# Performance work log

Measured on AMD Instinct MI355X. Metric: run time of the kernel, lower is better.

## Reference

```python
import jax, jax.numpy as jnp
import numpy as np

DIM = 768
NUM_HEADS = 12
HEAD_DIM = DIM // NUM_HEADS
SCALE = HEAD_DIM ** -0.5
B, N = 8, 1024


def setup_inputs() -> dict:
    key = jax.random.key(0)
    k1, k2, k3, k4 = jax.random.split(key, 4)
    s = 1.0 / np.sqrt(DIM)
    return {
        "x": jax.random.normal(k1, (B, N, DIM), dtype=jnp.float32),
        "w_qkv": jax.random.normal(k2, (DIM, 3 * DIM), dtype=jnp.float32) * s,  # qkv_bias=False
        "w_proj": jax.random.normal(k3, (DIM, DIM), dtype=jnp.float32) * s,
        "b_proj": jax.random.normal(k4, (DIM,), dtype=jnp.float32) * 0.01,
    }


def reference(x, w_qkv, w_proj, b_proj):
    Bb, Nn, C = x.shape
    qkv = x @ w_qkv  # [B, N, 3C]
    qkv = qkv.reshape(Bb, Nn, 3, NUM_HEADS, HEAD_DIM)
    q = qkv[:, :, 0].transpose(0, 2, 1, 3)  # [B, H, N, d]
    k = qkv[:, :, 1].transpose(0, 2, 1, 3)
    v = qkv[:, :, 2].transpose(0, 2, 1, 3)
    attn = jnp.einsum("bhqd,bhkd->bhqk", q, k) * SCALE
    attn = jax.nn.softmax(attn, axis=-1)  # dropout p=0 -> identity
    out = jnp.einsum("bhqk,bhkd->bhqd", attn, v)
    out = out.transpose(0, 2, 1, 3).reshape(Bb, Nn, C)
    return out @ w_proj + b_proj
```

## Files before the change

### kernel.cpp

```cpp
#include <hip/hip_runtime.h>
#include <stdint.h>

typedef __attribute__((ext_vector_type(8))) __bf16 bf16x8;
typedef __attribute__((ext_vector_type(8))) unsigned short u16x8;
typedef __attribute__((ext_vector_type(4))) unsigned short u16x4;
typedef __attribute__((ext_vector_type(4))) short s16x4;
typedef __attribute__((ext_vector_type(4))) float f32x4;

typedef unsigned int u32_as1 __attribute__((address_space(1)));
typedef unsigned int u32_as3 __attribute__((address_space(3)));

__device__ __forceinline__ unsigned short f2bf(float f) {
  unsigned int u = __float_as_uint(f);
  u += 0x7fffu + ((u >> 16) & 1u);
  return (unsigned short)(u >> 16);
}

__device__ __forceinline__ bf16x8 ld_frag(const unsigned short* p) {
  return __builtin_bit_cast(bf16x8, *(const u16x8*)p);
}

__device__ __forceinline__ f32x4 mfma16(s16x4 a, s16x4 b, f32x4 c) {
#if __has_builtin(__builtin_amdgcn_mfma_f32_16x16x16bf16_1k)
  return __builtin_amdgcn_mfma_f32_16x16x16bf16_1k(a, b, c, 0, 0, 0);
#elif __has_builtin(__builtin_amdgcn_mfma_f32_16x16x16_bf16_1k)
  return __builtin_amdgcn_mfma_f32_16x16x16_bf16_1k(a, b, c, 0, 0, 0);
#else
  asm volatile("v_mfma_f32_16x16x16_bf16 %0, %1, %2, %0"
               : "+v"(c) : "v"(a), "v"(b));
  return c;
#endif
}

__device__ __forceinline__ float fast_exp2(float x) {
#if __has_builtin(__builtin_amdgcn_exp2f)
  return __builtin_amdgcn_exp2f(x);
#else
  return exp2f(x);
#endif
}

__device__ __forceinline__ void async16(const void* g, void* l) {
  const u32_as1* gp = (const u32_as1*)(uintptr_t)g;
  u32_as3* lp = (u32_as3*)(uintptr_t)l;
  __builtin_amdgcn_global_load_lds(gp, lp, 16, 0, 0);
}

template <int N> __device__ __forceinline__ void wait_vmcnt() {
  if constexpr (N == 0)      asm volatile("s_waitcnt vmcnt(0)" ::: "memory");
  else if constexpr (N == 4) asm volatile("s_waitcnt vmcnt(4)" ::: "memory");
  else if constexpr (N == 6) asm volatile("s_waitcnt vmcnt(6)" ::: "memory");
}

__global__ __launch_bounds__(256) void prep_kernel(
    const float* __restrict__ x, const float* __restrict__ w_qkv,
    const float* __restrict__ w_proj, u16x4* __restrict__ x_bf,
    unsigned short* __restrict__ wqkvT, unsigned short* __restrict__ wprojT) {
  const int bid = blockIdx.x;
  const int t = threadIdx.x;
  if (bid < 6144) {
    const int i = bid * 256 + t;
    float4 v = ((const float4*)x)[i];
    u16x4 o;
    o[0] = f2bf(v.x); o[1] = f2bf(v.y); o[2] = f2bf(v.z); o[3] = f2bf(v.w);
    x_bf[i] = o;
    return;
  }
  __shared__ float tile[32][33];
  const float* w; unsigned short* wt; int N, bx, by;
  if (bid < 6144 + 1728) { const int r = bid - 6144; w = w_qkv; wt = wqkvT; N = 2304; bx = r % 72; by = r / 72; }
  else                   { const int r = bid - 7872; w = w_proj; wt = wprojT; N = 768; bx = r % 24; by = r / 24; }
  const int n0 = bx * 32, k0 = by * 32;
  const int tx = t & 31, ty = t >> 5;
#pragma unroll
  for (int r = 0; r < 4; r++)
    tile[ty + r * 8][tx] = w[(k0 + ty + r * 8) * N + n0 + tx];
  __syncthreads();
#pragma unroll
  for (int r = 0; r < 4; r++)
    wt[(n0 + ty + r * 8) * 768 + k0 + tx] = f2bf(tile[tx][ty + r * 8]);
}

template <int EPI>
__global__ __launch_bounds__(512, 2) void gemm256(
    const unsigned short* __restrict__ A, const unsigned short* __restrict__ Bt,
    unsigned short* __restrict__ qb, unsigned short* __restrict__ kb,
    unsigned short* __restrict__ vtb, float* __restrict__ outp,
    const float* __restrict__ bias) {
  constexpr int NKT = 12;
  constexpr int SSH = 24576;
  __shared__ unsigned short smem[3 * SSH];

  const int t = threadIdx.x;
  const int lane = t & 63, w = t >> 6;
  const int quad = lane >> 4, l15 = lane & 15;
  const int wm = w >> 1, wn = w & 1;

  const int bid = blockIdx.x;
  const int xcd = bid & 7, slot = bid >> 3;
  const int m0 = (xcd * 4 + (slot & 3)) * 256;
  const int n0 = (slot >> 2) * 128;

  int aoff[4][2], boff[4][2];
#pragma unroll
  for (int i = 0; i < 4; i++) {
    const int row = wm * 64 + i * 16 + l15;
    const int rs = row & 7;
#pragma unroll
    for (int kk = 0; kk < 2; kk++)
      aoff[i][kk] = row * 64 + (((kk * 4 + quad) ^ rs) << 3);
  }
#pragma unroll
  for (int j = 0; j < 4; j++) {
    const int row = wn * 64 + j * 16 + l15;
    const int rs = row & 7;
#pragma unroll
    for (int kk = 0; kk < 2; kk++)
      boff[j][kk] = 16384 + row * 64 + (((kk * 4 + quad) ^ rs) << 3);
  }

  const int srow = t >> 3;
  const int gch = ((t & 7) ^ (srow & 7)) << 3;
  const unsigned short* Ags = A + (m0 + srow) * 768 + gch;
  const unsigned short* Bgs = Bt + (n0 + srow) * 768 + gch;

  f32x4 acc[4][4];
  const f32x4 fzero = {0.f, 0.f, 0.f, 0.f};
#pragma unroll
  for (int i = 0; i < 4; i++)
#pragma unroll
    for (int j = 0; j < 4; j++) acc[i][j] = fzero;

  auto stage = [&](int kt, int part) {
    unsigned short* s = smem + (kt % 3) * SSH + t * 8;
    const int ko = kt * 64;
    if (part == 0) {
      async16(Ags + ko, s);
      async16(Ags + 49152 + ko, s + 4096);
      async16(Ags + 98304 + ko, s + 8192);
    } else {
      async16(Ags + 147456 + ko, s + 12288);
      async16(Bgs + ko, s + 16384);
      async16(Bgs + 49152 + ko, s + 20480);
    }
  };

  stage(0, 0); stage(0, 1);
  stage(1, 0); stage(1, 1);

#pragma unroll
  for (int kt = 0; kt < NKT; ++kt) {
    const unsigned short* S = smem + (kt % 3) * SSH;
#pragma unroll
    for (int ph = 0; ph < 2; ++ph) {
      if (ph == 0) {
        if (kt < NKT - 1) wait_vmcnt<6>();
        else              wait_vmcnt<0>();
      }
      __builtin_amdgcn_s_barrier();

      bf16x8 af[4], bf[4];
#pragma unroll
      for (int i = 0; i < 4; i++) af[i] = ld_frag(S + aoff[i][ph]);
#pragma unroll
      for (int j = 0; j < 4; j++) bf[j] = ld_frag(S + boff[j][ph]);

      if (kt + 2 < NKT) stage(kt + 2, ph);

      __builtin_amdgcn_s_setprio(1);
#pragma unroll
      for (int i = 0; i < 4; i++)
#pragma unroll
        for (int j = 0; j < 4; j++)
          acc[i][j] = __builtin_amdgcn_mfma_f32_16x16x32_bf16(af[i], bf[j], acc[i][j], 0, 0, 0);
      __builtin_amdgcn_s_setprio(0);
    }
  }

#pragma unroll
  for (int i = 0; i < 4; i++) {
    const int gmb = m0 + wm * 64 + i * 16 + quad * 4;
#pragma unroll
    for (int j = 0; j < 4; j++) {
      const int gc = n0 + wn * 64 + j * 16 + l15;
#pragma unroll
      for (int r = 0; r < 4; r++) {
        const int gm = gmb + r;
        float v = acc[i][j][r];
        if (EPI == 0) {
          const int b = gm >> 10, tok = gm & 1023;
          const int which = (gc >= 1536) ? 2 : (gc >= 768 ? 1 : 0);
          const int rem = gc - which * 768;
          const int h = rem >> 6, d = rem & 63;
          const int bh = b * 12 + h;
          const unsigned short bv = f2bf(v);
          if (which == 0)      qb[(bh << 16) + (tok << 6) + d] = bv;
          else if (which == 1) kb[(bh << 16) + (tok << 6) + d] = bv;
          else                 vtb[(bh << 16) + (d << 10) + tok] = bv;
        } else {
          outp[gm * 768 + gc] = v + bias[gc];
        }
      }
    }
  }
}

#define SWZC(row, c) (((row) << 6) + ((((c) + (row)) & 7) << 3))
#define C2 0.1803368801111244f

__global__ __launch_bounds__(256, 3) void attn_kernel(
    const unsigned short* __restrict__ qb, const unsigned short* __restrict__ kb,
    const unsigned short* __restrict__ vtb, unsigned short* __restrict__ aout) {
  __shared__ unsigned short smem[3 * 8192];

  const int t = threadIdx.x;
  const int lane = t & 63, w = t >> 6;
  const int quad = lane >> 4, l15 = lane & 15;
  const int bh = blockIdx.x;
  const int b = bh / 12, h = bh - b * 12;
  const int q0 = blockIdx.y * 128;
  const int base = bh << 16;

  bf16x8 qf[2][2];
#pragma unroll
  for (int qt = 0; qt < 2; qt++)
#pragma unroll
    for (int s = 0; s < 2; s++)
      qf[qt][s] = ld_frag(qb + base + ((q0 + w * 32 + qt * 16 + l15) << 6) +
                          s * 32 + quad * 8);

  f32x4 oacc[4][2];
  const f32x4 fzero = {0.f, 0.f, 0.f, 0.f};
#pragma unroll
  for (int dt = 0; dt < 4; dt++) { oacc[dt][0] = fzero; oacc[dt][1] = fzero; }
  float lsum0 = 0.f, lsum1 = 0.f;

  const int srow = t >> 3, schk = t & 7;
  const int c0 = ((schk - srow) & 7) * 8;
  const int c1 = ((schk - (srow + 32)) & 7) * 8;

  auto fillkv = [&](int tile, int buf) {
    const int kv0 = tile * 64;
    unsigned short* Ks = smem + buf * 8192;
    unsigned short* Vts = Ks + 4096;
    async16(kb + base + ((kv0 + srow) << 6) + c0, Ks + t * 8);
    async16(kb + base + ((kv0 + srow + 32) << 6) + c1, Ks + 2048 + t * 8);
    async16(vtb + base + (srow << 10) + kv0 + c0, Vts + t * 8);
    async16(vtb + base + ((srow + 32) << 10) + kv0 + c1, Vts + 2048 + t * 8);
  };

  fillkv(0, 0);
  fillkv(1, 1);
  int cur = 0;
  for (int it = 0; it < 16; ++it) {
    if (it < 15) wait_vmcnt<4>(); else wait_vmcnt<0>();
    asm volatile("s_barrier" ::: "memory");
    if (it + 2 < 16) {
      int tgt = cur + 2; if (tgt >= 3) tgt -= 3;
      fillkv(it + 2, tgt);
    }
    const unsigned short* Ks = smem + cur * 8192;
    const unsigned short* Vts = Ks + 4096;

    f32x4 st[4][2];
#pragma unroll
    for (int tc = 0; tc < 4; tc++) { st[tc][0] = fzero; st[tc][1] = fzero; }
#pragma unroll
    for (int s = 0; s < 2; s++) {
#pragma unroll
      for (int tc = 0; tc < 4; tc++) {
        const bf16x8 kf = ld_frag(Ks + SWZC(tc * 16 + l15, s * 4 + quad));
        st[tc][0] = __builtin_amdgcn_mfma_f32_16x16x32_bf16(kf, qf[0][s], st[tc][0], 0, 0, 0);
        st[tc][1] = __builtin_amdgcn_mfma_f32_16x16x32_bf16(kf, qf[1][s], st[tc][1], 0, 0, 0);
      }
    }

    s16x4 pf[4][2];
#pragma unroll
    for (int tc = 0; tc < 4; tc++) {
#pragma unroll
      for (int qt = 0; qt < 2; qt++) {
        const float p0 = fast_exp2(st[tc][qt][0] * C2);
        const float p1 = fast_exp2(st[tc][qt][1] * C2);
        const float p2 = fast_exp2(st[tc][qt][2] * C2);
        const float p3 = fast_exp2(st[tc][qt][3] * C2);
        const float ps = (p0 + p1) + (p2 + p3);
        if (qt == 0) lsum0 += ps; else lsum1 += ps;
        s16x4 pk;
        pk[0] = (short)f2bf(p0); pk[1] = (short)f2bf(p1);
        pk[2] = (short)f2bf(p2); pk[3] = (short)f2bf(p3);
        pf[tc][qt] = pk;
      }
    }

#pragma unroll
    for (int tc = 0; tc < 4; tc++) {
#pragma unroll
      for (int dt = 0; dt < 4; dt++) {
        const int row = dt * 16 + l15;
        const int addr = (row << 6) + ((((tc * 2 + (quad >> 1)) + row) & 7) << 3) +
                         ((quad & 1) << 2);
        const s16x4 vf = *(const s16x4*)(Vts + addr);
        oacc[dt][0] = mfma16(vf, pf[tc][0], oacc[dt][0]);
        oacc[dt][1] = mfma16(vf, pf[tc][1], oacc[dt][1]);
      }
    }

    cur += 1; if (cur == 3) cur = 0;
  }

  lsum0 += __shfl_xor(lsum0, 16); lsum0 += __shfl_xor(lsum0, 32);
  lsum1 += __shfl_xor(lsum1, 16); lsum1 += __shfl_xor(lsum1, 32);
  const float inv0 = 1.f / lsum0, inv1 = 1.f / lsum1;

  __syncthreads();
  unsigned short* Ot = smem;
#pragma unroll
  for (int dt = 0; dt < 4; dt++) {
#pragma unroll
    for (int qt = 0; qt < 2; qt++) {
      const float inv = qt == 0 ? inv0 : inv1;
      const int qrow = (w * 32 + qt * 16 + l15) * 72 + dt * 16 + quad * 4;
#pragma unroll
      for (int r = 0; r < 4; r++)
        Ot[qrow + r] = f2bf(oacc[dt][qt][r] * inv);
    }
  }
  __syncthreads();
#pragma unroll
  for (int it = 0; it < 4; it++) {
    const int q = it * 32 + (t >> 3);
    const int d0 = (t & 7) * 8;
    const u16x8 v = *(const u16x8*)(Ot + q * 72 + d0);
    *(u16x8*)(aout + (b * 1024 + q0 + q) * 768 + h * 64 + d0) = v;
  }
}

extern "C" void kernel_launch(void* const* d_in, const int* in_sizes, int n_in,
                              void* d_out, int out_size, void* d_ws, size_t ws_size,
                              hipStream_t stream) {
  (void)in_sizes; (void)n_in; (void)out_size; (void)ws_size;
  const float* x = (const float*)d_in[0];
  const float* w_qkv = (const float*)d_in[1];
  const float* w_proj = (const float*)d_in[2];
  const float* b_proj = (const float*)d_in[3];
  float* out = (float*)d_out;

  char* ws = (char*)d_ws;
  unsigned short* x_bf   = (unsigned short*)(ws);
  unsigned short* wqkvT  = (unsigned short*)(ws + 12582912);
  unsigned short* wprojT = (unsigned short*)(ws + 16121856);
  unsigned short* qb     = (unsigned short*)(ws + 17301504);
  unsigned short* kb     = (unsigned short*)(ws + 29884416);
  unsigned short* vtb    = (unsigned short*)(ws + 42467328);
  unsigned short* aout   = x_bf;

  prep_kernel<<<8448, 256, 0, stream>>>(x, w_qkv, w_proj, (u16x4*)x_bf, wqkvT, wprojT);
  gemm256<0><<<576, 512, 0, stream>>>(x_bf, wqkvT, qb, kb, vtb, nullptr, nullptr);
  attn_kernel<<<dim3(96, 8), 256, 0, stream>>>(qb, kb, vtb, aout);
  gemm256<1><<<192, 512, 0, stream>>>(aout, wprojT, nullptr, nullptr, nullptr, out, b_proj);
}
```

Before: 184.8 us.

## Retile GEMMs to 128x192 blocks with single-phase K pipeline

Changes both GEMMs from 256x128 output tiles to 128x192 tiles, with a 2x4 wave layout where each wave computes 64x48. This raises block counts from 576/192 to 768/256 to improve fill across CUs. The two-phase staging per K-tile becomes one stage of five async loads per K-tile with a single barrier, and the vmcnt wait is adjusted to match. The QKV epilogue now computes the q/k/v selection once per block. The trade-off is lower arithmetic intensity per block and more redundant A/B loads overall.

```diff
diff --git a/kernel.cpp b/kernel.cpp
--- a/kernel.cpp
+++ b/kernel.cpp
@@ -49,7 +49,7 @@
 template <int N> __device__ __forceinline__ void wait_vmcnt() {
   if constexpr (N == 0)      asm volatile("s_waitcnt vmcnt(0)" ::: "memory");
   else if constexpr (N == 4) asm volatile("s_waitcnt vmcnt(4)" ::: "memory");
-  else if constexpr (N == 6) asm volatile("s_waitcnt vmcnt(6)" ::: "memory");
+  else if constexpr (N == 5) asm volatile("s_waitcnt vmcnt(5)" ::: "memory");
 }
 
 __global__ __launch_bounds__(256) void prep_kernel(
@@ -82,123 +82,110 @@
 }
 
 template <int EPI>
-__global__ __launch_bounds__(512, 2) void gemm256(
+__global__ __launch_bounds__(512, 2) void gemm128(
     const unsigned short* __restrict__ A, const unsigned short* __restrict__ Bt,
     unsigned short* __restrict__ qb, unsigned short* __restrict__ kb,
     unsigned short* __restrict__ vtb, float* __restrict__ outp,
     const float* __restrict__ bias) {
   constexpr int NKT = 12;
-  constexpr int SSH = 24576;
+  constexpr int SSH = 20480;
   __shared__ unsigned short smem[3 * SSH];
 
   const int t = threadIdx.x;
   const int lane = t & 63, w = t >> 6;
   const int quad = lane >> 4, l15 = lane & 15;
-  const int wm = w >> 1, wn = w & 1;
+  const int wm = w >> 2, wn = w & 3;
 
   const int bid = blockIdx.x;
   const int xcd = bid & 7, slot = bid >> 3;
-  const int m0 = (xcd * 4 + (slot & 3)) * 256;
-  const int n0 = (slot >> 2) * 128;
-
-  int aoff[4][2], boff[4][2];
-#pragma unroll
-  for (int i = 0; i < 4; i++) {
-    const int row = wm * 64 + i * 16 + l15;
-    const int rs = row & 7;
-#pragma unroll
-    for (int kk = 0; kk < 2; kk++)
-      aoff[i][kk] = row * 64 + (((kk * 4 + quad) ^ rs) << 3);
-  }
-#pragma unroll
-  for (int j = 0; j < 4; j++) {
-    const int row = wn * 64 + j * 16 + l15;
-    const int rs = row & 7;
-#pragma unroll
-    for (int kk = 0; kk < 2; kk++)
-      boff[j][kk] = 16384 + row * 64 + (((kk * 4 + quad) ^ rs) << 3);
-  }
+  const int m0 = (xcd * 8 + (slot & 7)) * 128;
+  const int n0 = (slot >> 3) * 192;
+
+  const int rs = l15 & 7;
+  int arow[4], brow[3], co[2];
+#pragma unroll
+  for (int i = 0; i < 4; i++) arow[i] = (wm * 64 + i * 16 + l15) * 64;
+#pragma unroll
+  for (int j = 0; j < 3; j++) brow[j] = 8192 + (wn * 48 + j * 16 + l15) * 64;
+#pragma unroll
+  for (int kk = 0; kk < 2; kk++) co[kk] = ((kk * 4 + quad) ^ rs) << 3;
 
   const int srow = t >> 3;
   const int gch = ((t & 7) ^ (srow & 7)) << 3;
   const unsigned short* Ags = A + (m0 + srow) * 768 + gch;
   const unsigned short* Bgs = Bt + (n0 + srow) * 768 + gch;
 
-  f32x4 acc[4][4];
+  f32x4 acc[4][3];
   const f32x4 fzero = {0.f, 0.f, 0.f, 0.f};
 #pragma unroll
   for (int i = 0; i < 4; i++)
 #pragma unroll
-    for (int j = 0; j < 4; j++) acc[i][j] = fzero;
-
-  auto stage = [&](int kt, int part) {
+    for (int j = 0; j < 3; j++) acc[i][j] = fzero;
+
+  auto stage = [&](int kt) {
     unsigned short* s = smem + (kt % 3) * SSH + t * 8;
     const int ko = kt * 64;
-    if (part == 0) {
-      async16(Ags + ko, s);
-      async16(Ags + 49152 + ko, s + 4096);
-      async16(Ags + 98304 + ko, s + 8192);
-    } else {
-      async16(Ags + 147456 + ko, s + 12288);
-      async16(Bgs + ko, s + 16384);
-      async16(Bgs + 49152 + ko, s + 20480);
-    }
+    async16(Ags + ko, s);
+    async16(Ags + 49152 + ko, s + 4096);
+    async16(Bgs + ko, s + 8192);
+    async16(Bgs + 49152 + ko, s + 12288);
+    async16(Bgs + 98304 + ko, s + 16384);
   };
 
-  stage(0, 0); stage(0, 1);
-  stage(1, 0); stage(1, 1);
+  stage(0);
+  stage(1);
 
 #pragma unroll
   for (int kt = 0; kt < NKT; ++kt) {
+    if (kt < NKT - 1) wait_vmcnt<5>();
+    else              wait_vmcnt<0>();
+    __builtin_amdgcn_s_barrier();
+
+    if (kt + 2 < NKT) stage(kt + 2);
+
     const unsigned short* S = smem + (kt % 3) * SSH;
-#pragma unroll
-    for (int ph = 0; ph < 2; ++ph) {
-      if (ph == 0) {
-        if (kt < NKT - 1) wait_vmcnt<6>();
-        else              wait_vmcnt<0>();
-      }
-      __builtin_amdgcn_s_barrier();
-
-      bf16x8 af[4], bf[4];
-#pragma unroll
-      for (int i = 0; i < 4; i++) af[i] = ld_frag(S + aoff[i][ph]);
-#pragma unroll
-      for (int j = 0; j < 4; j++) bf[j] = ld_frag(S + boff[j][ph]);
-
-      if (kt + 2 < NKT) stage(kt + 2, ph);
-
-      __builtin_amdgcn_s_setprio(1);
+    bf16x8 af[2][4], bfr[2][3];
+#pragma unroll
+    for (int kk = 0; kk < 2; kk++) {
+#pragma unroll
+      for (int i = 0; i < 4; i++) af[kk][i] = ld_frag(S + arow[i] + co[kk]);
+#pragma unroll
+      for (int j = 0; j < 3; j++) bfr[kk][j] = ld_frag(S + brow[j] + co[kk]);
+    }
+
+    __builtin_amdgcn_s_setprio(1);
+#pragma unroll
+    for (int kk = 0; kk < 2; kk++)
 #pragma unroll
       for (int i = 0; i < 4; i++)
 #pragma unroll
-        for (int j = 0; j < 4; j++)
-          acc[i][j] = __builtin_amdgcn_mfma_f32_16x16x32_bf16(af[i], bf[j], acc[i][j], 0, 0, 0);
-      __builtin_amdgcn_s_setprio(0);
-    }
-  }
-
+        for (int j = 0; j < 3; j++)
+          acc[i][j] = __builtin_amdgcn_mfma_f32_16x16x32_bf16(af[kk][i], bfr[kk][j], acc[i][j], 0, 0, 0);
+    __builtin_amdgcn_s_setprio(0);
+  }
+
+  const int which = (n0 >= 1536) ? 2 : (n0 >= 768 ? 1 : 0);
+  const int cwb = n0 - which * 768 + wn * 48;
 #pragma unroll
   for (int i = 0; i < 4; i++) {
     const int gmb = m0 + wm * 64 + i * 16 + quad * 4;
 #pragma unroll
-    for (int j = 0; j < 4; j++) {
-      const int gc = n0 + wn * 64 + j * 16 + l15;
+    for (int j = 0; j < 3; j++) {
+      const int cw = cwb + j * 16 + l15;
 #pragma unroll
       for (int r = 0; r < 4; r++) {
         const int gm = gmb + r;
         float v = acc[i][j][r];
         if (EPI == 0) {
           const int b = gm >> 10, tok = gm & 1023;
-          const int which = (gc >= 1536) ? 2 : (gc >= 768 ? 1 : 0);
-          const int rem = gc - which * 768;
-          const int h = rem >> 6, d = rem & 63;
+          const int h = cw >> 6, d = cw & 63;
           const int bh = b * 12 + h;
           const unsigned short bv = f2bf(v);
           if (which == 0)      qb[(bh << 16) + (tok << 6) + d] = bv;
           else if (which == 1) kb[(bh << 16) + (tok << 6) + d] = bv;
           else                 vtb[(bh << 16) + (d << 10) + tok] = bv;
         } else {
-          outp[gm * 768 + gc] = v + bias[gc];
+          outp[gm * 768 + n0 + wn * 48 + j * 16 + l15] = v + bias[n0 + wn * 48 + j * 16 + l15];
         }
       }
     }
@@ -356,7 +343,7 @@
   unsigned short* aout   = x_bf;
 
   prep_kernel<<<8448, 256, 0, stream>>>(x, w_qkv, w_proj, (u16x4*)x_bf, wqkvT, wprojT);
-  gemm256<0><<<576, 512, 0, stream>>>(x_bf, wqkvT, qb, kb, vtb, nullptr, nullptr);
+  gemm128<0><<<768, 512, 0, stream>>>(x_bf, wqkvT, qb, kb, vtb, nullptr, nullptr);
   attn_kernel<<<dim3(96, 8), 256, 0, stream>>>(qb, kb, vtb, aout);
-  gemm256<1><<<192, 512, 0, stream>>>(aout, wprojT, nullptr, nullptr, nullptr, out, b_proj);
-}
+  gemm128<1><<<256, 512, 0, stream>>>(aout, wprojT, nullptr, nullptr, nullptr, out, b_proj);
+}
```

Result: no change. 186.9 us (+1.1%).
